# Performance work log

Hardware: AMD Instinct MI355X
Metric: run time of the kernel (lower is better)

Reference implementation:

```python
import jax, jax.numpy as jnp
import numpy as np

B, S, D, H, HD = 2, 2048, 1024, 16, 64
SCALE = HD ** (-0.5)

def setup_inputs() -> dict:
    key = jax.random.key(0)
    ks = jax.random.split(key, 11)
    f = jax.random.normal
    return {
        "K_in": f(ks[0], (B, S, D), jnp.float32),
        "V_in": f(ks[1], (B, S, D), jnp.float32),
        "Q_in": f(ks[2], (B, S, D), jnp.float32),
        "Wk": f(ks[3], (H, D, HD), jnp.float32) * 0.02,
        "bk": f(ks[4], (H, HD), jnp.float32) * 0.02,
        "Wq": f(ks[5], (H, D, HD), jnp.float32) * 0.02,
        "bq": f(ks[6], (H, HD), jnp.float32) * 0.02,
        "Wv": f(ks[7], (H, D, HD), jnp.float32) * 0.02,
        "bv": f(ks[8], (H, HD), jnp.float32) * 0.02,
        "Wp": f(ks[9], (D, D), jnp.float32) * 0.02,
        "bp": f(ks[10], (D,), jnp.float32) * 0.02,
    }

def reference(K_in, V_in, Q_in, Wk, bk, Wq, bq, Wv, bv, Wp, bp):
    # Per-head linear projections (batched over heads): [B,H,S,HD]
    K = jnp.einsum('bsd,hde->bhse', K_in, Wk) + bk[None, :, None, :]
    Q = jnp.einsum('bsd,hde->bhse', Q_in, Wq) + bq[None, :, None, :]
    V = jnp.einsum('bsd,hde->bhse', V_in, Wv) + bv[None, :, None, :]
    # Attention scores [B,H,S,S], softmax over keys
    W = jax.nn.softmax(jnp.einsum('bhqe,bhke->bhqk', Q, K) * SCALE, axis=-1)
    val = jnp.einsum('bhqk,bhke->bhqe', W, V)            # [B,H,S,HD]
    # Concatenate heads along feature dim -> [B,S,H*HD] = [B,S,D]
    concat = jnp.transpose(val, (0, 2, 1, 3)).reshape(K_in.shape[0], K_in.shape[1], -1)
    return concat @ Wp.T + bp
```

## Files before the change

kernel.cpp:

```cpp
#include <hip/hip_runtime.h>
#include <hip/hip_bf16.h>
#include <math.h>

typedef float f32x4 __attribute__((ext_vector_type(4)));
typedef short s16x8 __attribute__((ext_vector_type(8)));
typedef unsigned short us16x4 __attribute__((ext_vector_type(4)));
typedef unsigned short us16x8 __attribute__((ext_vector_type(8)));
typedef unsigned int u32x2 __attribute__((ext_vector_type(2)));

#define MFMA16(a, b, c) __builtin_amdgcn_mfma_f32_16x16x32_bf16(a, b, c, 0, 0, 0)

static constexpr int B_ = 2, S_ = 2048, D_ = 1024, H_ = 16, HD_ = 64;
static constexpr float QSCALE = 0.125f * 1.44269504088896340736f;

__device__ __forceinline__ unsigned short f2bf(float f) {
    unsigned int u = __builtin_bit_cast(unsigned int, f);
    u += 0x7fffu + ((u >> 16) & 1);
    return (unsigned short)(u >> 16);
}

#if defined(__has_builtin) && __has_builtin(__builtin_amdgcn_cvt_pk_bf16_f32)
typedef __bf16 bf16x2v __attribute__((ext_vector_type(2)));
__device__ __forceinline__ unsigned int pk_bf16(float a, float b) {
    return __builtin_bit_cast(unsigned int, __builtin_amdgcn_cvt_pk_bf16_f32(a, b));
}
#else
__device__ __forceinline__ unsigned int pk_bf16(float a, float b) {
    return ((unsigned int)f2bf(a)) | (((unsigned int)f2bf(b)) << 16);
}
#endif

__device__ __forceinline__ void glds16(const unsigned short* g, unsigned short* l) {
    __builtin_amdgcn_global_load_lds(
        (const __attribute__((address_space(1))) void*)g,
        (__attribute__((address_space(3))) void*)l, 16, 0, 0);
}

__global__ __launch_bounds__(256) void conv3(const float* __restrict__ s0,
                                             const float* __restrict__ s1,
                                             const float* __restrict__ s2,
                                             unsigned short* __restrict__ d0,
                                             unsigned short* __restrict__ d1,
                                             unsigned short* __restrict__ d2) {
    const int z = blockIdx.z;
    const float* src = (z == 0) ? s0 : (z == 1) ? s1 : s2;
    unsigned short* dst = (z == 0) ? d0 : (z == 1) ? d1 : d2;
    int i = (blockIdx.x * 256 + threadIdx.x) * 8;
    f32x4 a = *(const f32x4*)&src[i];
    f32x4 b = *(const f32x4*)&src[i + 4];
    s16x8 o;
#pragma unroll
    for (int j = 0; j < 4; j++) { o[j] = (short)f2bf(a[j]); o[4 + j] = (short)f2bf(b[j]); }
    *(s16x8*)&dst[i] = o;
}

__global__ __launch_bounds__(256) void conv_bf16(const float* __restrict__ src,
                                                 unsigned short* __restrict__ dst) {
    int i = (blockIdx.x * 256 + threadIdx.x) * 8;
    f32x4 a = *(const f32x4*)&src[i];
    f32x4 b = *(const f32x4*)&src[i + 4];
    s16x8 o;
#pragma unroll
    for (int j = 0; j < 4; j++) { o[j] = (short)f2bf(a[j]); o[4 + j] = (short)f2bf(b[j]); }
    *(s16x8*)&dst[i] = o;
}

__global__ __launch_bounds__(256) void transpose_w3(const float* __restrict__ W0,
                                                    const float* __restrict__ W1,
                                                    const float* __restrict__ W2,
                                                    unsigned short* __restrict__ Wt3) {
    const int z = blockIdx.z;
    const float* W = (z == 0) ? W0 : (z == 1) ? W1 : W2;
    unsigned short* dst = Wt3 + ((size_t)z << 20);
    const int h = blockIdx.x >> 2, dg = blockIdx.x & 3;
    const int lane = threadIdx.x & 63, w = threadIdx.x >> 6;
    const float* Wh = W + ((size_t)h << 16);
#pragma unroll
    for (int it = 0; it < 8; it++) {
        int d0 = dg * 256 + it * 32 + w * 8;
        us16x8 o;
#pragma unroll
        for (int j = 0; j < 8; j++) o[j] = f2bf(Wh[(d0 + j) * 64 + lane]);
        *(us16x8*)&dst[(size_t)(h * 64 + lane) * 1024 + d0] = o;
    }
}

__device__ __forceinline__ void gemm_core128(const unsigned short* __restrict__ A,
                                             const unsigned short* __restrict__ Bt,
                                             unsigned short* As, unsigned short* Bs,
                                             int m0, int n0, f32x4 acc[4][4]) {
    const int tid = threadIdx.x;
    const int lane = tid & 63;
    const int w = tid >> 6, wm = w & 1, wn = w >> 1;
    const int l16 = lane & 15, quad = lane >> 4;
    const int srow = tid >> 3;
    const int sg = (tid & 7) ^ (srow & 7);
    const unsigned short* Ag = A + (size_t)(m0 + srow) * 1024 + sg * 8;
    const unsigned short* Bg = Bt + (size_t)(n0 + srow) * 1024 + sg * 8;
    unsigned short* Al = As + tid * 8;
    unsigned short* Bl = Bs + tid * 8;
    const int xo = (l16 & 7);

    for (int k0 = 0; k0 < 1024; k0 += 64) {
        __syncthreads();
#pragma unroll
        for (int c = 0; c < 4; c++) {
            glds16(Ag + (size_t)c * 32 * 1024 + k0, Al + c * 2048);
            glds16(Bg + (size_t)c * 32 * 1024 + k0, Bl + c * 2048);
        }
        __syncthreads();
#pragma unroll
        for (int kc = 0; kc < 2; kc++) {
            s16x8 bf[4];
#pragma unroll
            for (int nt = 0; nt < 4; nt++)
                bf[nt] = *(const s16x8*)&Bs[(wn * 64 + nt * 16 + l16) * 64 +
                                            (((kc * 4 + quad) ^ xo) * 8)];
#pragma unroll
            for (int mt = 0; mt < 4; mt++) {
                s16x8 af = *(const s16x8*)&As[(wm * 64 + mt * 16 + l16) * 64 +
                                              (((kc * 4 + quad) ^ xo) * 8)];
#pragma unroll
                for (int nt = 0; nt < 4; nt++)
                    acc[mt][nt] = MFMA16(af, bf[nt], acc[mt][nt]);
            }
        }
    }
}

__global__ __launch_bounds__(256) void gemm_qkv(const unsigned short* __restrict__ Qc,
                                                const unsigned short* __restrict__ Kc,
                                                const unsigned short* __restrict__ Vc,
                                                const unsigned short* __restrict__ Wt3,
                                                const float* __restrict__ bq,
                                                const float* __restrict__ bk,
                                                const float* __restrict__ bv,
                                                unsigned short* __restrict__ Qr,
                                                unsigned short* __restrict__ Kr,
                                                unsigned short* __restrict__ Vt) {
    __shared__ unsigned short As[128 * 64];
    __shared__ unsigned short Bs[128 * 64];
    const int z = blockIdx.z;
    const unsigned short* A = (z == 0) ? Qc : (z == 1) ? Kc : Vc;
    const unsigned short* Bt = Wt3 + ((size_t)z << 20);
    const float* bias = (z == 0) ? bq : (z == 1) ? bk : bv;
    const int m0 = blockIdx.y * 128, n0 = blockIdx.x * 128;

    f32x4 acc[4][4] = {};
    gemm_core128(A, Bt, As, Bs, m0, n0, acc);

    const int tid = threadIdx.x;
    const int lane = tid & 63, w = tid >> 6;
    const int wm = w & 1, wn = w >> 1;
    const int l16 = lane & 15, quad = lane >> 4;
    const float scl = (z == 0) ? QSCALE : 1.0f;

    __syncthreads();
    unsigned short* T = ((w < 2) ? As : Bs) + (w & 1) * 4096;
#pragma unroll
    for (int mt = 0; mt < 4; mt++)
#pragma unroll
        for (int nt = 0; nt < 4; nt++) {
            int nl = nt * 16 + l16;
            float bsv = bias[n0 + wn * 64 + nl];
#pragma unroll
            for (int r = 0; r < 4; r++) {
                int ml = mt * 16 + quad * 4 + r;
                unsigned short val = f2bf((acc[mt][nt][r] + bsv) * scl);
                int row = (z == 2) ? nl : ml;
                int col = (z == 2) ? ml : nl;
                T[row * 64 + (((col >> 3) ^ (row & 7)) * 8) + (col & 7)] = val;
            }
        }
#pragma unroll
    for (int it = 0; it < 8; it++) {
        int rr = it * 8 + (lane >> 3);
        int g = lane & 7;
        us16x8 vv = *(const us16x8*)&T[rr * 64 + ((g ^ (rr & 7)) * 8)];
        if (z == 2) {
            int n = n0 + wn * 64 + rr;
            int mb = m0 + wm * 64 + g * 8;
            int b = mb >> 11, s = mb & 2047;
            *(us16x8*)&Vt[(((size_t)(b * H_ + (n >> 6))) * HD_ + (n & 63)) * S_ + s] = vv;
        } else {
            unsigned short* dst = z ? Kr : Qr;
            *(us16x8*)&dst[(size_t)(m0 + wm * 64 + rr) * 1024 + n0 + wn * 64 + g * 8] = vv;
        }
    }
}

__global__ __launch_bounds__(256) void gemm_out(const unsigned short* __restrict__ A,
                                                const unsigned short* __restrict__ Bt,
                                                const float* __restrict__ bias,
                                                float* __restrict__ C) {
    __shared__ unsigned short As[128 * 64];
    __shared__ unsigned short Bs[64 * 64];
    const int tid = threadIdx.x;
    const int lane = tid & 63;
    const int w = tid >> 6, wm = w & 1, wn = w >> 1;
    const int l16 = lane & 15, quad = lane >> 4;
    const int m0 = blockIdx.y * 128, n0 = blockIdx.x * 64;
    const int srow = tid >> 3;
    const int sg = (tid & 7) ^ (srow & 7);
    const unsigned short* Ag = A + (size_t)(m0 + srow) * 1024 + sg * 8;
    const unsigned short* Bg = Bt + (size_t)(n0 + srow) * 1024 + sg * 8;
    unsigned short* Al = As + tid * 8;
    unsigned short* Bl = Bs + tid * 8;
    const int xo = l16 & 7;

    f32x4 acc[4][2] = {};
    for (int k0 = 0; k0 < 1024; k0 += 64) {
        __syncthreads();
#pragma unroll
        for (int c = 0; c < 4; c++)
            glds16(Ag + (size_t)c * 32 * 1024 + k0, Al + c * 2048);
#pragma unroll
        for (int c = 0; c < 2; c++)
            glds16(Bg + (size_t)c * 32 * 1024 + k0, Bl + c * 2048);
        __syncthreads();
#pragma unroll
        for (int kc = 0; kc < 2; kc++) {
            s16x8 bf[2];
#pragma unroll
            for (int nt = 0; nt < 2; nt++)
                bf[nt] = *(const s16x8*)&Bs[(wn * 32 + nt * 16 + l16) * 64 +
                                            (((kc * 4 + quad) ^ xo) * 8)];
#pragma unroll
            for (int mt = 0; mt < 4; mt++) {
                s16x8 af = *(const s16x8*)&As[(wm * 64 + mt * 16 + l16) * 64 +
                                              (((kc * 4 + quad) ^ xo) * 8)];
#pragma unroll
                for (int nt = 0; nt < 2; nt++)
                    acc[mt][nt] = MFMA16(af, bf[nt], acc[mt][nt]);
            }
        }
    }
    const int lq = quad;
#pragma unroll
    for (int mt = 0; mt < 4; mt++)
#pragma unroll
        for (int nt = 0; nt < 2; nt++)
#pragma unroll
            for (int r = 0; r < 4; r++) {
                int mg = m0 + wm * 64 + mt * 16 + lq * 4 + r;
                int ng = n0 + wn * 32 + nt * 16 + l16;
                C[(size_t)mg * 1024 + ng] = acc[mt][nt][r] + bias[ng];
            }
}

__global__ __launch_bounds__(256) void flash_attn(const unsigned short* __restrict__ Qr,
                                                  const unsigned short* __restrict__ Kr,
                                                  const unsigned short* __restrict__ Vt,
                                                  unsigned short* __restrict__ Cc) {
    __shared__ unsigned short Ks[64 * 64];
    __shared__ unsigned short Vs[64 * 64];
    constexpr int LDT = 72;
    __shared__ unsigned short P4[4][16 * LDT];

    const int tid = threadIdx.x;
    const int lane = tid & 63, w = tid >> 6;
    const int l16 = lane & 15, quad = lane >> 4;
    const int bh = blockIdx.x, q0 = blockIdx.y * 64;
    const int b = bh >> 4, h = bh & 15;
    const int s_q = q0 + w * 16 + l16;

    const unsigned short* Qp = Qr + ((size_t)(b * S_ + s_q)) * D_ + h * HD_;
    s16x8 aq0 = *(const s16x8*)&Qp[quad * 8];
    s16x8 aq1 = *(const s16x8*)&Qp[32 + quad * 8];

    const int srow = tid >> 3;
    const int sg = (tid & 7) ^ (srow & 7);
    const unsigned short* kg = Kr + ((size_t)(b * S_ + srow)) * D_ + h * HD_ + sg * 8;
    const unsigned short* vg = Vt + (((size_t)(b * H_ + h)) * HD_ + srow) * S_ + sg * 8;
    unsigned short* Kl = Ks + tid * 8;
    unsigned short* Vl = Vs + tid * 8;
    unsigned short* Pw = P4[w];
    const int pbase = l16 * LDT + quad * 4;
    const int xo = l16 & 7;

    float l_part = 0.f;
    f32x4 o[4] = {};
    const f32x4 z4 = {0.f, 0.f, 0.f, 0.f};

    for (int k0 = 0; k0 < S_; k0 += 64) {
        __syncthreads();
        glds16(kg, Kl);
        glds16(kg + (size_t)32 * D_, Kl + 2048);
        glds16(vg, Vl);
        glds16(vg + (size_t)32 * S_, Vl + 2048);
        kg += (size_t)64 * D_;
        vg += 64;
        __syncthreads();

#pragma unroll
        for (int g = 0; g < 4; g++) {
            int row = g * 16 + l16;
            s16x8 kb0 = *(const s16x8*)&Ks[row * 64 + ((quad ^ xo) * 8)];
            s16x8 kb1 = *(const s16x8*)&Ks[row * 64 + (((4 + quad) ^ xo) * 8)];
            f32x4 sc = MFMA16(kb0, aq0, z4);
            sc = MFMA16(kb1, aq1, sc);
            float e0 = exp2f(sc[0]), e1 = exp2f(sc[1]);
            float e2 = exp2f(sc[2]), e3 = exp2f(sc[3]);
            l_part += (e0 + e1) + (e2 + e3);
            u32x2 pv;
            pv[0] = pk_bf16(e0, e1);
            pv[1] = pk_bf16(e2, e3);
            *(u32x2*)&Pw[pbase + g * 16] = pv;
        }
        s16x8 pB0 = *(const s16x8*)&Pw[l16 * LDT + quad * 8];
        s16x8 pB1 = *(const s16x8*)&Pw[l16 * LDT + 32 + quad * 8];
#pragma unroll
        for (int t = 0; t < 4; t++) {
            int row = t * 16 + l16;
            s16x8 v0 = *(const s16x8*)&Vs[row * 64 + ((quad ^ xo) * 8)];
            s16x8 v1 = *(const s16x8*)&Vs[row * 64 + (((4 + quad) ^ xo) * 8)];
            o[t] = MFMA16(v0, pB0, o[t]);
            o[t] = MFMA16(v1, pB1, o[t]);
        }
    }
    float l = l_part;
    l += __shfl_xor(l, 16);
    l += __shfl_xor(l, 32);
    float rinv = 1.0f / l;
    unsigned short* Cp = Cc + ((size_t)(b * S_ + s_q)) * D_ + h * HD_;
#pragma unroll
    for (int t = 0; t < 4; t++) {
        u32x2 ov;
        ov[0] = pk_bf16(o[t][0] * rinv, o[t][1] * rinv);
        ov[1] = pk_bf16(o[t][2] * rinv, o[t][3] * rinv);
        *(u32x2*)&Cp[t * 16 + quad * 4] = ov;
    }
}

extern "C" void kernel_launch(void* const* d_in, const int* in_sizes, int n_in,
                              void* d_out, int out_size, void* d_ws, size_t ws_size,
                              hipStream_t stream) {
    const float* K_in = (const float*)d_in[0];
    const float* V_in = (const float*)d_in[1];
    const float* Q_in = (const float*)d_in[2];
    const float* Wk   = (const float*)d_in[3];
    const float* bk   = (const float*)d_in[4];
    const float* Wq   = (const float*)d_in[5];
    const float* bq   = (const float*)d_in[6];
    const float* Wv   = (const float*)d_in[7];
    const float* bv   = (const float*)d_in[8];
    const float* Wp   = (const float*)d_in[9];
    const float* bp   = (const float*)d_in[10];

    unsigned short* ws16 = (unsigned short*)d_ws;
    const size_t MC = 1u << 20;
    unsigned short* Qc  = ws16;
    unsigned short* Kc  = Qc + 4 * MC;
    unsigned short* Vc  = Kc + 4 * MC;
    unsigned short* Wt3 = Vc + 4 * MC;
    unsigned short* Qr  = Wt3 + 3 * MC;
    unsigned short* Kr  = Qr + 4 * MC;
    unsigned short* Vt  = Kr + 4 * MC;
    unsigned short* Cc  = Qc;
    unsigned short* Wpb = Wt3;

    conv3<<<dim3(2048, 1, 3), 256, 0, stream>>>(Q_in, K_in, V_in, Qc, Kc, Vc);
    transpose_w3<<<dim3(64, 1, 3), 256, 0, stream>>>(Wq, Wk, Wv, Wt3);

    gemm_qkv<<<dim3(8, 32, 3), 256, 0, stream>>>(Qc, Kc, Vc, Wt3, bq, bk, bv, Qr, Kr, Vt);

    conv_bf16<<<512, 256, 0, stream>>>(Wp, Wpb);

    flash_attn<<<dim3(32, 32), 256, 0, stream>>>(Qr, Kr, Vt, Cc);

    gemm_out<<<dim3(16, 32), 256, 0, stream>>>(Cc, Wpb, bp, (float*)d_out);
}
```

Before: 256.0 us.

## Double-buffer K/V tiles in flash attention to overlap loads with compute

The K and V shared-memory tiles become two buffers. The next tile's global-to-LDS loads are issued right after a single barrier and before the current tile's QK/PV MFMA work, instead of bracketing synchronous loads between two barriers. This hides global memory latency behind compute and drops one barrier per iteration. The cost is double the K/V LDS footprint, which could lower occupancy, and correctness now depends on the barrier waiting for the outstanding async LDS loads. An unused alias in the projection GEMM epilogue is also removed.

```diff
diff --git a/kernel.cpp b/kernel.cpp
--- a/kernel.cpp
+++ b/kernel.cpp
@@ -235,14 +235,13 @@
             }
         }
     }
-    const int lq = quad;
 #pragma unroll
     for (int mt = 0; mt < 4; mt++)
 #pragma unroll
         for (int nt = 0; nt < 2; nt++)
 #pragma unroll
             for (int r = 0; r < 4; r++) {
-                int mg = m0 + wm * 64 + mt * 16 + lq * 4 + r;
+                int mg = m0 + wm * 64 + mt * 16 + quad * 4 + r;
                 int ng = n0 + wn * 32 + nt * 16 + l16;
                 C[(size_t)mg * 1024 + ng] = acc[mt][nt][r] + bias[ng];
             }
@@ -252,8 +251,8 @@
                                                   const unsigned short* __restrict__ Kr,
                                                   const unsigned short* __restrict__ Vt,
                                                   unsigned short* __restrict__ Cc) {
-    __shared__ unsigned short Ks[64 * 64];
-    __shared__ unsigned short Vs[64 * 64];
+    __shared__ unsigned short Ks[2][64 * 64];
+    __shared__ unsigned short Vs[2][64 * 64];
     constexpr int LDT = 72;
     __shared__ unsigned short P4[4][16 * LDT];
 
@@ -272,8 +271,10 @@
     const int sg = (tid & 7) ^ (srow & 7);
     const unsigned short* kg = Kr + ((size_t)(b * S_ + srow)) * D_ + h * HD_ + sg * 8;
     const unsigned short* vg = Vt + (((size_t)(b * H_ + h)) * HD_ + srow) * S_ + sg * 8;
-    unsigned short* Kl = Ks + tid * 8;
-    unsigned short* Vl = Vs + tid * 8;
+    unsigned short* Kl0 = &Ks[0][tid * 8];
+    unsigned short* Kl1 = &Ks[1][tid * 8];
+    unsigned short* Vl0 = &Vs[0][tid * 8];
+    unsigned short* Vl1 = &Vs[1][tid * 8];
     unsigned short* Pw = P4[w];
     const int pbase = l16 * LDT + quad * 4;
     const int xo = l16 & 7;
@@ -282,21 +283,32 @@
     f32x4 o[4] = {};
     const f32x4 z4 = {0.f, 0.f, 0.f, 0.f};
 
+    glds16(kg, Kl0);
+    glds16(kg + (size_t)32 * D_, Kl0 + 2048);
+    glds16(vg, Vl0);
+    glds16(vg + (size_t)32 * S_, Vl0 + 2048);
+
     for (int k0 = 0; k0 < S_; k0 += 64) {
-        __syncthreads();
-        glds16(kg, Kl);
-        glds16(kg + (size_t)32 * D_, Kl + 2048);
-        glds16(vg, Vl);
-        glds16(vg + (size_t)32 * S_, Vl + 2048);
-        kg += (size_t)64 * D_;
-        vg += 64;
-        __syncthreads();
+        const int cur = (k0 >> 6) & 1;
+        __syncthreads();
+        if (k0 + 64 < S_) {
+            const unsigned short* kn = kg + (size_t)(k0 + 64) * D_;
+            const unsigned short* vn = vg + (k0 + 64);
+            unsigned short* Kln = cur ? Kl0 : Kl1;
+            unsigned short* Vln = cur ? Vl0 : Vl1;
+            glds16(kn, Kln);
+            glds16(kn + (size_t)32 * D_, Kln + 2048);
+            glds16(vn, Vln);
+            glds16(vn + (size_t)32 * S_, Vln + 2048);
+        }
+        const unsigned short* Ksc = Ks[cur];
+        const unsigned short* Vsc = Vs[cur];
 
 #pragma unroll
         for (int g = 0; g < 4; g++) {
             int row = g * 16 + l16;
-            s16x8 kb0 = *(const s16x8*)&Ks[row * 64 + ((quad ^ xo) * 8)];
-            s16x8 kb1 = *(const s16x8*)&Ks[row * 64 + (((4 + quad) ^ xo) * 8)];
+            s16x8 kb0 = *(const s16x8*)&Ksc[row * 64 + ((quad ^ xo) * 8)];
+            s16x8 kb1 = *(const s16x8*)&Ksc[row * 64 + (((4 + quad) ^ xo) * 8)];
             f32x4 sc = MFMA16(kb0, aq0, z4);
             sc = MFMA16(kb1, aq1, sc);
             float e0 = exp2f(sc[0]), e1 = exp2f(sc[1]);
@@ -312,8 +324,8 @@
 #pragma unroll
         for (int t = 0; t < 4; t++) {
             int row = t * 16 + l16;
-            s16x8 v0 = *(const s16x8*)&Vs[row * 64 + ((quad ^ xo) * 8)];
-            s16x8 v1 = *(const s16x8*)&Vs[row * 64 + (((4 + quad) ^ xo) * 8)];
+            s16x8 v0 = *(const s16x8*)&Vsc[row * 64 + ((quad ^ xo) * 8)];
+            s16x8 v1 = *(const s16x8*)&Vsc[row * 64 + (((4 + quad) ^ xo) * 8)];
             o[t] = MFMA16(v0, pB0, o[t]);
             o[t] = MFMA16(v1, pB1, o[t]);
         }
```

Result: slower. 263.7 us (+3.0%).

## Double-buffer LDS in shared GEMM core, shrink QKV tile, use fast exp2

Applied to the files above, without the earlier changes.

Replaces the single-buffered GEMM main loop with a double-buffered one that prefetches the next K-slice into a second LDS buffer while the current one is consumed, removing one barrier per iteration. The QKV projection switches from 128x128 to 128x64 tiles, doubling its grid for more parallelism, and gemm_out now reuses the same core. The epilogue is rewritten with padded LDS staging. Flash attention calls the hardware exp2 builtin instead of exp2f. The risks are that async LDS loads may not be complete at the single barrier, and that the smaller tiles reload the A operand more often.

```diff
diff --git a/kernel.cpp b/kernel.cpp
--- a/kernel.cpp
+++ b/kernel.cpp
@@ -28,6 +28,12 @@
 __device__ __forceinline__ unsigned int pk_bf16(float a, float b) {
     return ((unsigned int)f2bf(a)) | (((unsigned int)f2bf(b)) << 16);
 }
+#endif
+
+#if defined(__has_builtin) && __has_builtin(__builtin_amdgcn_exp2f)
+__device__ __forceinline__ float fast_exp2(float x) { return __builtin_amdgcn_exp2f(x); }
+#else
+__device__ __forceinline__ float fast_exp2(float x) { return exp2f(x); }
 #endif
 
 __device__ __forceinline__ void glds16(const unsigned short* g, unsigned short* l) {
@@ -85,10 +91,10 @@
     }
 }
 
-__device__ __forceinline__ void gemm_core128(const unsigned short* __restrict__ A,
+__device__ __forceinline__ void gemm_core_db(const unsigned short* __restrict__ A,
                                              const unsigned short* __restrict__ Bt,
-                                             unsigned short* As, unsigned short* Bs,
-                                             int m0, int n0, f32x4 acc[4][4]) {
+                                             unsigned short* lds,
+                                             int m0, int n0, f32x4 acc[4][2]) {
     const int tid = threadIdx.x;
     const int lane = tid & 63;
     const int w = tid >> 6, wm = w & 1, wn = w >> 1;
@@ -97,31 +103,42 @@
     const int sg = (tid & 7) ^ (srow & 7);
     const unsigned short* Ag = A + (size_t)(m0 + srow) * 1024 + sg * 8;
     const unsigned short* Bg = Bt + (size_t)(n0 + srow) * 1024 + sg * 8;
-    unsigned short* Al = As + tid * 8;
-    unsigned short* Bl = Bs + tid * 8;
-    const int xo = (l16 & 7);
+    const int xo = l16 & 7;
+    unsigned short* AsBuf[2] = { lds, lds + 12288 };
+    unsigned short* BsBuf[2] = { lds + 8192, lds + 20480 };
+
+#pragma unroll
+    for (int c = 0; c < 4; c++) glds16(Ag + (size_t)c * 32 * 1024, AsBuf[0] + tid * 8 + c * 2048);
+#pragma unroll
+    for (int c = 0; c < 2; c++) glds16(Bg + (size_t)c * 32 * 1024, BsBuf[0] + tid * 8 + c * 2048);
 
     for (int k0 = 0; k0 < 1024; k0 += 64) {
+        const int cur = (k0 >> 6) & 1;
         __syncthreads();
-#pragma unroll
-        for (int c = 0; c < 4; c++) {
-            glds16(Ag + (size_t)c * 32 * 1024 + k0, Al + c * 2048);
-            glds16(Bg + (size_t)c * 32 * 1024 + k0, Bl + c * 2048);
-        }
-        __syncthreads();
+        if (k0 + 64 < 1024) {
+            const int nxt = cur ^ 1;
+#pragma unroll
+            for (int c = 0; c < 4; c++)
+                glds16(Ag + (size_t)c * 32 * 1024 + k0 + 64, AsBuf[nxt] + tid * 8 + c * 2048);
+#pragma unroll
+            for (int c = 0; c < 2; c++)
+                glds16(Bg + (size_t)c * 32 * 1024 + k0 + 64, BsBuf[nxt] + tid * 8 + c * 2048);
+        }
+        const unsigned short* Asc = AsBuf[cur];
+        const unsigned short* Bsc = BsBuf[cur];
 #pragma unroll
         for (int kc = 0; kc < 2; kc++) {
-            s16x8 bf[4];
-#pragma unroll
-            for (int nt = 0; nt < 4; nt++)
-                bf[nt] = *(const s16x8*)&Bs[(wn * 64 + nt * 16 + l16) * 64 +
-                                            (((kc * 4 + quad) ^ xo) * 8)];
+            s16x8 bf[2];
+#pragma unroll
+            for (int nt = 0; nt < 2; nt++)
+                bf[nt] = *(const s16x8*)&Bsc[(wn * 32 + nt * 16 + l16) * 64 +
+                                             (((kc * 4 + quad) ^ xo) * 8)];
 #pragma unroll
             for (int mt = 0; mt < 4; mt++) {
-                s16x8 af = *(const s16x8*)&As[(wm * 64 + mt * 16 + l16) * 64 +
-                                              (((kc * 4 + quad) ^ xo) * 8)];
-#pragma unroll
-                for (int nt = 0; nt < 4; nt++)
+                s16x8 af = *(const s16x8*)&Asc[(wm * 64 + mt * 16 + l16) * 64 +
+                                               (((kc * 4 + quad) ^ xo) * 8)];
+#pragma unroll
+                for (int nt = 0; nt < 2; nt++)
                     acc[mt][nt] = MFMA16(af, bf[nt], acc[mt][nt]);
             }
         }
@@ -138,53 +155,66 @@
                                                 unsigned short* __restrict__ Qr,
                                                 unsigned short* __restrict__ Kr,
                                                 unsigned short* __restrict__ Vt) {
-    __shared__ unsigned short As[128 * 64];
-    __shared__ unsigned short Bs[128 * 64];
+    __shared__ unsigned short lds[24576];
     const int z = blockIdx.z;
     const unsigned short* A = (z == 0) ? Qc : (z == 1) ? Kc : Vc;
     const unsigned short* Bt = Wt3 + ((size_t)z << 20);
     const float* bias = (z == 0) ? bq : (z == 1) ? bk : bv;
-    const int m0 = blockIdx.y * 128, n0 = blockIdx.x * 128;
-
-    f32x4 acc[4][4] = {};
-    gemm_core128(A, Bt, As, Bs, m0, n0, acc);
+    const int m0 = blockIdx.y * 128, n0 = blockIdx.x * 64;
+
+    f32x4 acc[4][2] = {};
+    gemm_core_db(A, Bt, lds, m0, n0, acc);
 
     const int tid = threadIdx.x;
     const int lane = tid & 63, w = tid >> 6;
     const int wm = w & 1, wn = w >> 1;
     const int l16 = lane & 15, quad = lane >> 4;
     const float scl = (z == 0) ? QSCALE : 1.0f;
-
-    __syncthreads();
-    unsigned short* T = ((w < 2) ? As : Bs) + (w & 1) * 4096;
-#pragma unroll
-    for (int mt = 0; mt < 4; mt++)
-#pragma unroll
-        for (int nt = 0; nt < 4; nt++) {
-            int nl = nt * 16 + l16;
-            float bsv = bias[n0 + wn * 64 + nl];
-#pragma unroll
-            for (int r = 0; r < 4; r++) {
-                int ml = mt * 16 + quad * 4 + r;
-                unsigned short val = f2bf((acc[mt][nt][r] + bsv) * scl);
-                int row = (z == 2) ? nl : ml;
-                int col = (z == 2) ? ml : nl;
-                T[row * 64 + (((col >> 3) ^ (row & 7)) * 8) + (col & 7)] = val;
+    unsigned short* T = lds + w * 2560;
+
+    if (z == 2) {
+#pragma unroll
+        for (int mt = 0; mt < 4; mt++)
+#pragma unroll
+            for (int nt = 0; nt < 2; nt++) {
+                int nl = nt * 16 + l16;
+                float bsv = bias[n0 + wn * 32 + nl];
+#pragma unroll
+                for (int r = 0; r < 4; r++) {
+                    int ml = mt * 16 + quad * 4 + r;
+                    T[nl * 72 + ml] = f2bf(acc[mt][nt][r] + bsv);
+                }
             }
-        }
-#pragma unroll
-    for (int it = 0; it < 8; it++) {
-        int rr = it * 8 + (lane >> 3);
-        int g = lane & 7;
-        us16x8 vv = *(const us16x8*)&T[rr * 64 + ((g ^ (rr & 7)) * 8)];
-        if (z == 2) {
-            int n = n0 + wn * 64 + rr;
+#pragma unroll
+        for (int it = 0; it < 4; it++) {
+            int rr = it * 8 + (lane >> 3);
+            int g = lane & 7;
+            us16x8 vv = *(const us16x8*)&T[rr * 72 + g * 8];
+            int n = n0 + wn * 32 + rr;
             int mb = m0 + wm * 64 + g * 8;
             int b = mb >> 11, s = mb & 2047;
             *(us16x8*)&Vt[(((size_t)(b * H_ + (n >> 6))) * HD_ + (n & 63)) * S_ + s] = vv;
-        } else {
-            unsigned short* dst = z ? Kr : Qr;
-            *(us16x8*)&dst[(size_t)(m0 + wm * 64 + rr) * 1024 + n0 + wn * 64 + g * 8] = vv;
+        }
+    } else {
+#pragma unroll
+        for (int mt = 0; mt < 4; mt++)
+#pragma unroll
+            for (int nt = 0; nt < 2; nt++) {
+                int nl = nt * 16 + l16;
+                float bsv = bias[n0 + wn * 32 + nl];
+#pragma unroll
+                for (int r = 0; r < 4; r++) {
+                    int ml = mt * 16 + quad * 4 + r;
+                    T[ml * 40 + nl] = f2bf((acc[mt][nt][r] + bsv) * scl);
+                }
+            }
+        unsigned short* dst = z ? Kr : Qr;
+#pragma unroll
+        for (int it = 0; it < 4; it++) {
+            int rr = it * 16 + (lane >> 2);
+            int g = lane & 3;
+            us16x8 vv = *(const us16x8*)&T[rr * 40 + g * 8];
+            *(us16x8*)&dst[(size_t)(m0 + wm * 64 + rr) * 1024 + n0 + wn * 32 + g * 8] = vv;
         }
     }
 }
@@ -193,56 +223,20 @@
                                                 const unsigned short* __restrict__ Bt,
                                                 const float* __restrict__ bias,
                                                 float* __restrict__ C) {
-    __shared__ unsigned short As[128 * 64];
-    __shared__ unsigned short Bs[64 * 64];
-    const int tid = threadIdx.x;
-    const int lane = tid & 63;
-    const int w = tid >> 6, wm = w & 1, wn = w >> 1;
+    __shared__ unsigned short lds[24576];
+    const int m0 = blockIdx.y * 128, n0 = blockIdx.x * 64;
+    f32x4 acc[4][2] = {};
+    gemm_core_db(A, Bt, lds, m0, n0, acc);
+    const int lane = threadIdx.x & 63, w = threadIdx.x >> 6;
+    const int wm = w & 1, wn = w >> 1;
     const int l16 = lane & 15, quad = lane >> 4;
-    const int m0 = blockIdx.y * 128, n0 = blockIdx.x * 64;
-    const int srow = tid >> 3;
-    const int sg = (tid & 7) ^ (srow & 7);
-    const unsigned short* Ag = A + (size_t)(m0 + srow) * 1024 + sg * 8;
-    const unsigned short* Bg = Bt + (size_t)(n0 + srow) * 1024 + sg * 8;
-    unsigned short* Al = As + tid * 8;
-    unsigned short* Bl = Bs + tid * 8;
-    const int xo = l16 & 7;
-
-    f32x4 acc[4][2] = {};
-    for (int k0 = 0; k0 < 1024; k0 += 64) {
-        __syncthreads();
-#pragma unroll
-        for (int c = 0; c < 4; c++)
-            glds16(Ag + (size_t)c * 32 * 1024 + k0, Al + c * 2048);
-#pragma unroll
-        for (int c = 0; c < 2; c++)
-            glds16(Bg + (size_t)c * 32 * 1024 + k0, Bl + c * 2048);
-        __syncthreads();
-#pragma unroll
-        for (int kc = 0; kc < 2; kc++) {
-            s16x8 bf[2];
-#pragma unroll
-            for (int nt = 0; nt < 2; nt++)
-                bf[nt] = *(const s16x8*)&Bs[(wn * 32 + nt * 16 + l16) * 64 +
-                                            (((kc * 4 + quad) ^ xo) * 8)];
-#pragma unroll
-            for (int mt = 0; mt < 4; mt++) {
-                s16x8 af = *(const s16x8*)&As[(wm * 64 + mt * 16 + l16) * 64 +
-                                              (((kc * 4 + quad) ^ xo) * 8)];
-#pragma unroll
-                for (int nt = 0; nt < 2; nt++)
-                    acc[mt][nt] = MFMA16(af, bf[nt], acc[mt][nt]);
-            }
-        }
-    }
-    const int lq = quad;
 #pragma unroll
     for (int mt = 0; mt < 4; mt++)
 #pragma unroll
         for (int nt = 0; nt < 2; nt++)
 #pragma unroll
             for (int r = 0; r < 4; r++) {
-                int mg = m0 + wm * 64 + mt * 16 + lq * 4 + r;
+                int mg = m0 + wm * 64 + mt * 16 + quad * 4 + r;
                 int ng = n0 + wn * 32 + nt * 16 + l16;
                 C[(size_t)mg * 1024 + ng] = acc[mt][nt][r] + bias[ng];
             }
@@ -299,8 +293,8 @@
             s16x8 kb1 = *(const s16x8*)&Ks[row * 64 + (((4 + quad) ^ xo) * 8)];
             f32x4 sc = MFMA16(kb0, aq0, z4);
             sc = MFMA16(kb1, aq1, sc);
-            float e0 = exp2f(sc[0]), e1 = exp2f(sc[1]);
-            float e2 = exp2f(sc[2]), e3 = exp2f(sc[3]);
+            float e0 = fast_exp2(sc[0]), e1 = fast_exp2(sc[1]);
+            float e2 = fast_exp2(sc[2]), e3 = fast_exp2(sc[3]);
             l_part += (e0 + e1) + (e2 + e3);
             u32x2 pv;
             pv[0] = pk_bf16(e0, e1);
@@ -362,7 +356,7 @@
     conv3<<<dim3(2048, 1, 3), 256, 0, stream>>>(Q_in, K_in, V_in, Qc, Kc, Vc);
     transpose_w3<<<dim3(64, 1, 3), 256, 0, stream>>>(Wq, Wk, Wv, Wt3);
 
-    gemm_qkv<<<dim3(8, 32, 3), 256, 0, stream>>>(Qc, Kc, Vc, Wt3, bq, bk, bv, Qr, Kr, Vt);
+    gemm_qkv<<<dim3(16, 32, 3), 256, 0, stream>>>(Qc, Kc, Vc, Wt3, bq, bk, bv, Qr, Kr, Vt);
 
     conv_bf16<<<512, 256, 0, stream>>>(Wp, Wpb);
 
```

Measured after the change: 262.3 us. 2.4% more time.
